# Optimization experiments

Hardware: AMD Instinct MI355X
Metric: run time of the kernel (lower is better)

## Reference

```python
import jax, jax.numpy as jnp
import numpy as np

D_MODEL = 1024
NUM_HEADS = 16
HEAD_DIM = D_MODEL // NUM_HEADS


def setup_inputs() -> dict:
    key = jax.random.key(0)
    k_x, k_wqkv, k_bqkv, k_wout, k_bout = jax.random.split(key, 5)
    B, S = 2, 2048
    x = jax.random.normal(k_x, (B, S, D_MODEL), dtype=jnp.float32)
    # haiku Linear: y = x @ W + b, W shape [in, out]
    init_scale = 1.0 / np.sqrt(D_MODEL)
    W_qkv = jax.random.normal(k_wqkv, (D_MODEL, 3 * D_MODEL), dtype=jnp.float32) * init_scale
    b_qkv = jnp.zeros((3 * D_MODEL,), dtype=jnp.float32)
    W_out = jax.random.normal(k_wout, (D_MODEL, D_MODEL), dtype=jnp.float32) * init_scale
    b_out = jnp.zeros((D_MODEL,), dtype=jnp.float32)
    return {"x": x, "W_qkv": W_qkv, "b_qkv": b_qkv, "W_out": W_out, "b_out": b_out}


def reference(x, W_qkv, b_qkv, W_out, b_out):
    B, S, _ = x.shape
    qkv = x @ W_qkv + b_qkv                      # [B, S, 3*D]
    q, k, v = jnp.split(qkv, 3, axis=-1)         # each [B, S, D]
    # [B, S, D] -> [B, H, S, Hd]
    def heads(t):
        return t.reshape(B, S, NUM_HEADS, HEAD_DIM).transpose(0, 2, 1, 3)
    q, k, v = heads(q), heads(k), heads(v)
    scale = jnp.sqrt(jnp.float32(HEAD_DIM)).astype(x.dtype)
    attn = jnp.einsum('bhqd,bhkd->bhqk', q, k) / scale   # [B, H, S, S]
    attn = jax.nn.softmax(attn, axis=-1)
    out = jnp.einsum('bhqk,bhkd->bhqd', attn, v)          # [B, H, S, Hd]
    out = out.transpose(0, 2, 1, 3).reshape(B, S, D_MODEL)
    return out @ W_out + b_out
```

## Files before the change

kernel.cpp:

```cpp
#include <hip/hip_runtime.h>
#include <stdint.h>


#define BATCH 2
#define SEQ 2048
#define DM 1024
#define NH 16
#define HD 64
#define M_TOT 4096
#define QSCALE 0.18033688011112042f

typedef __bf16 bf16x8 __attribute__((ext_vector_type(8)));
typedef __bf16 bf16x4 __attribute__((ext_vector_type(4)));
typedef float  f32x4  __attribute__((ext_vector_type(4)));

__device__ __forceinline__ void gld_lds16(const void* g, void* l) {
    __builtin_amdgcn_global_load_lds(
        (const __attribute__((address_space(1))) uint32_t*)g,
        (__attribute__((address_space(3))) uint32_t*)l, 16, 0, 0);
}

__launch_bounds__(256)
__global__ void prep_kernel(const float* __restrict__ x,
                            const float* __restrict__ Wqkv,
                            const float* __restrict__ Wout,
                            __bf16* __restrict__ xs,
                            __bf16* __restrict__ wqt,
                            __bf16* __restrict__ wot)
{
    __shared__ float T[64][69];
    const int tid = threadIdx.x;
    const int blk = blockIdx.x;

    if (blk < 4096) {
        const int i  = blk * 256 + tid;
        const int m  = i >> 8;
        const int c4 = (i & 255) * 4;
        float4 v = *reinterpret_cast<const float4*>(&x[(size_t)m * DM + c4]);
        float a[4] = {v.x, v.y, v.z, v.w};
        bf16x4 hi, lo;
        #pragma unroll
        for (int j = 0; j < 4; ++j) {
            __bf16 h = (__bf16)a[j];
            hi[j] = h;
            lo[j] = (__bf16)(a[j] - (float)h);
        }
        *reinterpret_cast<bf16x4*>(&xs[(size_t)m * (2*DM) + c4]) = hi;
        *reinterpret_cast<bf16x4*>(&xs[(size_t)m * (2*DM) + DM + c4]) = lo;
        return;
    }

    const int bb = (blk < 4864) ? blk - 4096 : blk - 4864;
    const float* W = (blk < 4864) ? Wqkv : Wout;
    __bf16* Wt     = (blk < 4864) ? wqt  : wot;
    const int N    = (blk < 4864) ? 3 * DM : DM;
    const int k0 = (bb & 15) * 64, n0 = (bb >> 4) * 64;

    {
        const int kr = tid >> 4, c4 = (tid & 15) * 4;
        #pragma unroll
        for (int i = 0; i < 4; ++i) {
            float4 v = *reinterpret_cast<const float4*>(
                &W[(size_t)(k0 + kr + 16 * i) * N + n0 + c4]);
            *reinterpret_cast<float4*>(&T[kr + 16 * i][c4]) = v;
        }
    }
    __syncthreads();
    {
        const int n = tid >> 2, kc = (tid & 3) * 16;
        __bf16 hi[16], lo[16];
        #pragma unroll
        for (int j = 0; j < 16; ++j) {
            float v = T[kc + j][n];
            __bf16 h = (__bf16)v;
            hi[j] = h;
            lo[j] = (__bf16)(v - (float)h);
        }
        const size_t ro = (size_t)(n0 + n) * (2*DM) + k0 + kc;
        *reinterpret_cast<bf16x8*>(&Wt[ro])          = *reinterpret_cast<bf16x8*>(&hi[0]);
        *reinterpret_cast<bf16x8*>(&Wt[ro + 8])      = *reinterpret_cast<bf16x8*>(&hi[8]);
        *reinterpret_cast<bf16x8*>(&Wt[ro + DM])     = *reinterpret_cast<bf16x8*>(&lo[0]);
        *reinterpret_cast<bf16x8*>(&Wt[ro + DM + 8]) = *reinterpret_cast<bf16x8*>(&lo[8]);
    }
}

__launch_bounds__(512, 2)
__global__ void gemm_qkv_kernel(const __bf16* __restrict__ A,
                                const __bf16* __restrict__ Bt,
                                const float* __restrict__ bias,
                                __bf16* __restrict__ qs,
                                __bf16* __restrict__ khi_g,
                                __bf16* __restrict__ klo_g,
                                __bf16* __restrict__ vt_g)
{
    __shared__ __align__(16) __bf16 pool[65536];

    const int tid  = threadIdx.x;
    const int w    = tid >> 6;
    const int lane = tid & 63;
    const int n16  = lane & 15;
    const int quad = lane >> 4;

    const int wg = (blockIdx.x & 7) * 24 + (blockIdx.x >> 3);
    const int bm = (wg & 15) * 256;
    const int bn = (wg >> 4) * 256;

    const int wm = (w >> 2) * 128;
    const int wn = (w & 3) * 64;

    const int r0 = tid >> 3;
    const int c0 = ((tid & 7) ^ (r0 & 7));

    auto stage = [&](int p, int kcol, int nbuf) {
        __bf16* dst = pool + nbuf * 32768 + p * 8192;
        const __bf16* gsrc = (p < 2)
            ? A  + (size_t)(bm + p * 128) * (2*DM) + kcol
            : Bt + (size_t)(bn + (p - 2) * 128) * (2*DM) + kcol;
        gld_lds16(gsrc + (size_t)r0 * (2*DM) + c0 * 8,        dst + (size_t)tid * 8);
        gld_lds16(gsrc + (size_t)(r0 + 64) * (2*DM) + c0 * 8, dst + (size_t)(512 + tid) * 8);
    };

    const int rowA = (wm + n16) * 64;
    const int rowB = (wn + n16) * 64;
    const int sx0 = ((quad)     ^ (n16 & 7)) << 3;
    const int sx1 = ((4 + quad) ^ (n16 & 7)) << 3;

    f32x4 acc[8][4] = {};
    bf16x8 af[4][2], bf0[2][2], bf1[2][2];

    stage(0, 0, 0); stage(1, 0, 0); stage(2, 0, 0); stage(3, 0, 0);

    #pragma unroll 2
    for (int t = 0; t < 48; ++t) {
        const int buf = t & 1;
        const __bf16* bufA = pool + buf * 32768;
        const __bf16* bufB = bufA + 16384;
        const int nbuf = buf ^ 1;
        const bool pre = (t < 47);
        const int tt = t + 1;
        const int a_k = (tt < 16) ? tt * 64 : tt * 64 - DM;
        const int b_k = (tt < 32) ? tt * 64 : tt * 64 - 2 * DM;

        if (pre) {
            stage(0, a_k, nbuf);
            asm volatile("s_waitcnt vmcnt(2)" ::: "memory");
        } else {
            asm volatile("s_waitcnt vmcnt(0)" ::: "memory");
        }
        __builtin_amdgcn_s_barrier();
        __builtin_amdgcn_sched_barrier(0);
        #pragma unroll
        for (int i = 0; i < 4; ++i) {
            af[i][0] = *reinterpret_cast<const bf16x8*>(bufA + rowA + i * 1024 + sx0);
            af[i][1] = *reinterpret_cast<const bf16x8*>(bufA + rowA + i * 1024 + sx1);
        }
        #pragma unroll
        for (int j = 0; j < 2; ++j) {
            bf0[j][0] = *reinterpret_cast<const bf16x8*>(bufB + rowB + j * 1024 + sx0);
            bf0[j][1] = *reinterpret_cast<const bf16x8*>(bufB + rowB + j * 1024 + sx1);
        }
        asm volatile("s_waitcnt lgkmcnt(0)" ::: "memory");
        __builtin_amdgcn_sched_barrier(0);
        __builtin_amdgcn_s_setprio(1);
        #pragma unroll
        for (int i = 0; i < 4; ++i)
            #pragma unroll
            for (int j = 0; j < 2; ++j) {
                acc[i][j] = __builtin_amdgcn_mfma_f32_16x16x32_bf16(af[i][0], bf0[j][0], acc[i][j], 0, 0, 0);
                acc[i][j] = __builtin_amdgcn_mfma_f32_16x16x32_bf16(af[i][1], bf0[j][1], acc[i][j], 0, 0, 0);
            }
        __builtin_amdgcn_s_setprio(0);

        #pragma unroll
        for (int j = 0; j < 2; ++j) {
            bf1[j][0] = *reinterpret_cast<const bf16x8*>(bufB + rowB + (2 + j) * 1024 + sx0);
            bf1[j][1] = *reinterpret_cast<const bf16x8*>(bufB + rowB + (2 + j) * 1024 + sx1);
        }
        if (pre) stage(1, a_k, nbuf);
        __builtin_amdgcn_s_barrier();
        __builtin_amdgcn_sched_barrier(0);
        asm volatile("s_waitcnt lgkmcnt(0)" ::: "memory");
        __builtin_amdgcn_sched_barrier(0);
        __builtin_amdgcn_s_setprio(1);
        #pragma unroll
        for (int i = 0; i < 4; ++i)
            #pragma unroll
            for (int j = 0; j < 2; ++j) {
                acc[i][2 + j] = __builtin_amdgcn_mfma_f32_16x16x32_bf16(af[i][0], bf1[j][0], acc[i][2 + j], 0, 0, 0);
                acc[i][2 + j] = __builtin_amdgcn_mfma_f32_16x16x32_bf16(af[i][1], bf1[j][1], acc[i][2 + j], 0, 0, 0);
            }
        __builtin_amdgcn_s_setprio(0);

        #pragma unroll
        for (int i = 0; i < 4; ++i) {
            af[i][0] = *reinterpret_cast<const bf16x8*>(bufA + rowA + (4 + i) * 1024 + sx0);
            af[i][1] = *reinterpret_cast<const bf16x8*>(bufA + rowA + (4 + i) * 1024 + sx1);
        }
        if (pre) stage(2, b_k, nbuf);
        __builtin_amdgcn_s_barrier();
        __builtin_amdgcn_sched_barrier(0);
        asm volatile("s_waitcnt lgkmcnt(0)" ::: "memory");
        __builtin_amdgcn_sched_barrier(0);
        __builtin_amdgcn_s_setprio(1);
        #pragma unroll
        for (int i = 0; i < 4; ++i)
            #pragma unroll
            for (int j = 0; j < 2; ++j) {
                acc[4 + i][j] = __builtin_amdgcn_mfma_f32_16x16x32_bf16(af[i][0], bf0[j][0], acc[4 + i][j], 0, 0, 0);
                acc[4 + i][j] = __builtin_amdgcn_mfma_f32_16x16x32_bf16(af[i][1], bf0[j][1], acc[4 + i][j], 0, 0, 0);
            }
        __builtin_amdgcn_s_setprio(0);

        if (pre) stage(3, b_k, nbuf);
        __builtin_amdgcn_s_barrier();
        __builtin_amdgcn_sched_barrier(0);
        __builtin_amdgcn_s_setprio(1);
        #pragma unroll
        for (int i = 0; i < 4; ++i)
            #pragma unroll
            for (int j = 0; j < 2; ++j) {
                acc[4 + i][2 + j] = __builtin_amdgcn_mfma_f32_16x16x32_bf16(af[i][0], bf1[j][0], acc[4 + i][2 + j], 0, 0, 0);
                acc[4 + i][2 + j] = __builtin_amdgcn_mfma_f32_16x16x32_bf16(af[i][1], bf1[j][1], acc[4 + i][2 + j], 0, 0, 0);
            }
        __builtin_amdgcn_s_setprio(0);
    }

    __syncthreads();

    const int colb = bn + wn;
    const int part = colb >> 10;
    const int hh   = (colb & 1023) >> 6;

    float bv[4];
    #pragma unroll
    for (int j = 0; j < 4; ++j) bv[j] = bias[colb + j * 16 + n16];

    __bf16* scrH = pool + w * 4608;
    __bf16* scrL = scrH + 2304;
    const int lr = lane & 31, hc = lane >> 5;

    #pragma unroll
    for (int mi = 0; mi < 2; ++mi) {
        const int brow = bm + wm + mi * 64;
        const int b    = brow >> 11;
        const int s0   = brow & 2047;
        const int bh   = b * NH + hh;
        const int kt   = s0 >> 6;
        const size_t tb = ((size_t)bh * 32 + kt) * 4096;

        #pragma unroll
        for (int p = 0; p < 2; ++p) {
            if (part == 2) {
                #pragma unroll
                for (int jj = 0; jj < 2; ++jj) {
                    const int j = 2 * p + jj;
                    #pragma unroll
                    for (int i = 0; i < 4; ++i) {
                        bf16x4 v4;
                        #pragma unroll
                        for (int r = 0; r < 4; ++r)
                            v4[r] = (__bf16)(acc[4 * mi + i][j][r] + bv[j]);
                        *reinterpret_cast<bf16x4*>(
                            &scrH[(jj * 16 + n16) * 72 + i * 16 + quad * 4]) = v4;
                    }
                }
            } else {
                #pragma unroll
                for (int ii = 0; ii < 2; ++ii) {
                    const int i = 2 * p + ii;
                    #pragma unroll
                    for (int j = 0; j < 4; ++j) {
                        #pragma unroll
                        for (int r = 0; r < 4; ++r) {
                            float val = acc[4 * mi + i][j][r] + bv[j];
                            if (part == 0) val *= QSCALE;
                            __bf16 h = (__bf16)val;
                            const int so = (ii * 16 + quad * 4 + r) * 72 + j * 16 + n16;
                            scrH[so] = h;
                            scrL[so] = (__bf16)(val - (float)h);
                        }
                    }
                }
            }
            __syncthreads();

            if (part == 0) {
                const size_t qbase = ((size_t)bh * SEQ + s0 + 32 * p + lr) * 128;
                #pragma unroll
                for (int t = 0; t < 4; ++t) {
                    const int ch = hc * 4 + t;
                    *reinterpret_cast<bf16x8*>(&qs[qbase + ch * 8]) =
                        *reinterpret_cast<const bf16x8*>(&scrH[lr * 72 + ch * 8]);
                    *reinterpret_cast<bf16x8*>(&qs[qbase + 64 + ch * 8]) =
                        *reinterpret_cast<const bf16x8*>(&scrL[lr * 72 + ch * 8]);
                }
            } else if (part == 1) {
                const int kr = 32 * p + lr;
                #pragma unroll
                for (int t = 0; t < 4; ++t) {
                    const int ch = hc * 4 + t;
                    const int src = (ch ^ (lr & 7)) * 8;
                    *reinterpret_cast<bf16x8*>(&khi_g[tb + kr * 64 + ch * 8]) =
                        *reinterpret_cast<const bf16x8*>(&scrH[lr * 72 + src]);
                    *reinterpret_cast<bf16x8*>(&klo_g[tb + kr * 64 + ch * 8]) =
                        *reinterpret_cast<const bf16x8*>(&scrL[lr * 72 + src]);
                }
            } else {
                const int d = 32 * p + lr;
                #pragma unroll
                for (int t = 0; t < 4; ++t) {
                    const int ch = hc * 4 + t;
                    const int src = (ch ^ (lr & 7)) * 8;
                    *reinterpret_cast<bf16x8*>(&vt_g[tb + d * 64 + ch * 8]) =
                        *reinterpret_cast<const bf16x8*>(&scrH[lr * 72 + src]);
                }
            }
            __syncthreads();
        }
    }
}

__launch_bounds__(256)
__global__ void gemm_out_kernel(const __bf16* __restrict__ A,
                                const __bf16* __restrict__ Bt,
                                const float* __restrict__ bias,
                                float* __restrict__ out)
{
    __shared__ __align__(16) __bf16 AsH[128 * 32];
    __shared__ __align__(16) __bf16 AsL[128 * 32];
    __shared__ __align__(16) __bf16 BsH[64 * 32];
    __shared__ __align__(16) __bf16 BsL[64 * 32];

    const int tid  = threadIdx.x;
    const int w    = tid >> 6;
    const int lane = tid & 63;
    const int n16  = lane & 15;
    const int quad = lane >> 4;
    const int bm = blockIdx.x * 128, bn = blockIdx.y * 64;
    const int wm = (w & 1) * 64,     wn = (w >> 1) * 32;

    const int srow = tid >> 2, sc = (tid & 3) * 8;
    const __bf16* Ar = A  + (size_t)(bm + srow) * (2*DM) + sc;
    const __bf16* Br = Bt + (size_t)(bn + srow) * (2*DM) + sc;

    f32x4 acc[4][2] = {};

    for (int k0 = 0; k0 < DM; k0 += 32) {
        __syncthreads();
        gld_lds16(Ar + k0,                         &AsH[(size_t)tid * 8]);
        gld_lds16(Ar + k0 + (size_t)64*2*DM,       &AsH[(size_t)(256 + tid) * 8]);
        gld_lds16(Ar + DM + k0,                    &AsL[(size_t)tid * 8]);
        gld_lds16(Ar + DM + k0 + (size_t)64*2*DM,  &AsL[(size_t)(256 + tid) * 8]);
        gld_lds16(Br + k0,                         &BsH[(size_t)tid * 8]);
        gld_lds16(Br + DM + k0,                    &BsL[(size_t)tid * 8]);
        __syncthreads();

        bf16x8 afh[4], afl[4], bfh[2], bfl[2];
        #pragma unroll
        for (int i = 0; i < 4; ++i) {
            const int ro = (wm + i*16 + n16) * 32 + quad * 8;
            afh[i] = *reinterpret_cast<const bf16x8*>(&AsH[ro]);
            afl[i] = *reinterpret_cast<const bf16x8*>(&AsL[ro]);
        }
        #pragma unroll
        for (int j = 0; j < 2; ++j) {
            const int ro = (wn + j*16 + n16) * 32 + quad * 8;
            bfh[j] = *reinterpret_cast<const bf16x8*>(&BsH[ro]);
            bfl[j] = *reinterpret_cast<const bf16x8*>(&BsL[ro]);
        }
        #pragma unroll
        for (int i = 0; i < 4; ++i)
            #pragma unroll
            for (int j = 0; j < 2; ++j) {
                acc[i][j] = __builtin_amdgcn_mfma_f32_16x16x32_bf16(afh[i], bfh[j], acc[i][j], 0, 0, 0);
                acc[i][j] = __builtin_amdgcn_mfma_f32_16x16x32_bf16(afh[i], bfl[j], acc[i][j], 0, 0, 0);
                acc[i][j] = __builtin_amdgcn_mfma_f32_16x16x32_bf16(afl[i], bfh[j], acc[i][j], 0, 0, 0);
            }
    }

    #pragma unroll
    for (int j = 0; j < 2; ++j) {
        const int col = bn + wn + j * 16 + n16;
        const float bvv = bias[col];
        #pragma unroll
        for (int i = 0; i < 4; ++i) {
            const int row0 = bm + wm + i * 16 + quad * 4;
            #pragma unroll
            for (int r = 0; r < 4; ++r)
                out[(size_t)(row0 + r) * DM + col] = acc[i][j][r] + bvv;
        }
    }
}

__launch_bounds__(512, 1)
__global__ void flash_attn_v7_kernel(const __bf16* __restrict__ qs,
                                     const __bf16* __restrict__ khi_g,
                                     const __bf16* __restrict__ klo_g,
                                     const __bf16* __restrict__ vt_g,
                                     __bf16* __restrict__ ctx2)
{
    __shared__ __align__(16) __bf16 Khi[2][4096];
    __shared__ __align__(16) __bf16 Klo[2][4096];
    __shared__ __align__(16) __bf16 Vt [2][4096];
    __shared__ __align__(16) __bf16 Ps [16384];

    const int tid  = threadIdx.x;
    const int w    = tid >> 6;
    const int lane = tid & 63;
    const int n16  = lane & 15;
    const int quad = lane >> 4;
    const int wgid = (blockIdx.x & 7) * 32 + (blockIdx.x >> 3);
    const int bh = wgid >> 3;
    const int qt = wgid & 7;

    bf16x8 qh[2][2], ql[2][2];
    #pragma unroll
    for (int qg = 0; qg < 2; ++qg) {
        const size_t qrow =
            ((size_t)bh * SEQ + qt * 256 + w * 32 + qg * 16 + n16) * 128;
        #pragma unroll
        for (int s2 = 0; s2 < 2; ++s2) {
            qh[qg][s2] = *reinterpret_cast<const bf16x8*>(&qs[qrow + s2 * 32 + quad * 8]);
            ql[qg][s2] = *reinterpret_cast<const bf16x8*>(&qs[qrow + 64 + s2 * 32 + quad * 8]);
        }
    }

    f32x4 o[2][4] = {};
    float l_lane[2] = {};

    for (int kt2 = 0; kt2 < 16; ++kt2) {
        __syncthreads();
        {
            const int buf = w >> 2;
            const size_t tb = ((size_t)bh * 32 + kt2 * 2 + buf) * 4096;
            #pragma unroll
            for (int t = 0; t < 6; ++t) {
                const int rem = (w & 3) * 6 + t;
                const int arr = rem >> 3, sub = rem & 7;
                const int eo = sub * 512 + lane * 8;
                const __bf16* g = (arr == 0 ? khi_g : arr == 1 ? klo_g : vt_g) + tb + eo;
                __bf16* l = (arr == 0 ? Khi[buf] : arr == 1 ? Klo[buf] : Vt[buf]) + eo;
                gld_lds16(g, l);
            }
        }
        __syncthreads();

        #pragma unroll
        for (int hf = 0; hf < 2; ++hf) {
            const __bf16* KhiB = Khi[hf];
            const __bf16* KloB = Klo[hf];
            const __bf16* VtB  = Vt[hf];

            #pragma unroll
            for (int kg = 0; kg < 4; ++kg) {
                const int r = kg * 16 + n16;
                const int o0 = r * 64 + ((quad ^ (r & 7)) << 3);
                const int o1 = r * 64 + (((4 + quad) ^ (r & 7)) << 3);
                bf16x8 kh0 = *reinterpret_cast<const bf16x8*>(&KhiB[o0]);
                bf16x8 kl0 = *reinterpret_cast<const bf16x8*>(&KloB[o0]);
                bf16x8 kh1 = *reinterpret_cast<const bf16x8*>(&KhiB[o1]);
                bf16x8 kl1 = *reinterpret_cast<const bf16x8*>(&KloB[o1]);
                #pragma unroll
                for (int qg = 0; qg < 2; ++qg) {
                    f32x4 sa = {}, sb = {};
                    sa = __builtin_amdgcn_mfma_f32_16x16x32_bf16(kh0, qh[qg][0], sa, 0, 0, 0);
                    sb = __builtin_amdgcn_mfma_f32_16x16x32_bf16(kh1, qh[qg][1], sb, 0, 0, 0);
                    sa = __builtin_amdgcn_mfma_f32_16x16x32_bf16(kl0, qh[qg][0], sa, 0, 0, 0);
                    sb = __builtin_amdgcn_mfma_f32_16x16x32_bf16(kl1, qh[qg][1], sb, 0, 0, 0);
                    sa = __builtin_amdgcn_mfma_f32_16x16x32_bf16(kh0, ql[qg][0], sa, 0, 0, 0);
                    sb = __builtin_amdgcn_mfma_f32_16x16x32_bf16(kh1, ql[qg][1], sb, 0, 0, 0);
                    f32x4 st = sa + sb;

                    f32x4 pp;
                    #pragma unroll
                    for (int r2 = 0; r2 < 4; ++r2) pp[r2] = exp2f(st[r2]);
                    l_lane[qg] += (pp[0] + pp[1]) + (pp[2] + pp[3]);

                    bf16x4 p4;
                    #pragma unroll
                    for (int r2 = 0; r2 < 4; ++r2) p4[r2] = (__bf16)pp[r2];
                    const int prow = w * 32 + qg * 16 + n16;
                    const int ch2 = kg * 2 + (quad >> 1);
                    const int off = prow * 64 + ((ch2 ^ (prow & 7)) << 3) + (quad & 1) * 4;
                    *reinterpret_cast<bf16x4*>(&Ps[off]) = p4;
                }
            }

            bf16x8 pa[2][2];
            #pragma unroll
            for (int qg = 0; qg < 2; ++qg) {
                const int prow = w * 32 + qg * 16 + n16;
                #pragma unroll
                for (int s2 = 0; s2 < 2; ++s2)
                    pa[qg][s2] = *reinterpret_cast<const bf16x8*>(
                        &Ps[prow * 64 + (((s2 * 4 + quad) ^ (prow & 7)) << 3)]);
            }
            #pragma unroll
            for (int c = 0; c < 4; ++c) {
                const int vr = c * 16 + n16;
                bf16x8 vb0 = *reinterpret_cast<const bf16x8*>(
                    &VtB[vr * 64 + ((quad ^ (vr & 7)) << 3)]);
                bf16x8 vb1 = *reinterpret_cast<const bf16x8*>(
                    &VtB[vr * 64 + (((4 + quad) ^ (vr & 7)) << 3)]);
                #pragma unroll
                for (int qg = 0; qg < 2; ++qg) {
                    o[qg][c] = __builtin_amdgcn_mfma_f32_16x16x32_bf16(pa[qg][0], vb0, o[qg][c], 0, 0, 0);
                    o[qg][c] = __builtin_amdgcn_mfma_f32_16x16x32_bf16(pa[qg][1], vb1, o[qg][c], 0, 0, 0);
                }
            }
        }
    }

    #pragma unroll
    for (int qg = 0; qg < 2; ++qg) {
        l_lane[qg] += __shfl_xor(l_lane[qg], 16, 64);
        l_lane[qg] += __shfl_xor(l_lane[qg], 32, 64);
    }

    const int b = bh >> 4, hh = bh & 15;
    #pragma unroll
    for (int qg = 0; qg < 2; ++qg) {
        #pragma unroll
        for (int r2 = 0; r2 < 4; ++r2) {
            const float l = __shfl(l_lane[qg], (quad << 4) + quad * 4 + r2, 64);
            const float linv = 1.0f / l;
            const int srow = qt * 256 + w * 32 + qg * 16 + quad * 4 + r2;
            const size_t rowoff = (size_t)(b * SEQ + srow) * (2*DM);
            #pragma unroll
            for (int c = 0; c < 4; ++c) {
                const int col = hh * HD + c * 16 + n16;
                float v = o[qg][c][r2] * linv;
                __bf16 h = (__bf16)v;
                ctx2[rowoff + col] = h;
                ctx2[rowoff + DM + col] = (__bf16)(v - (float)h);
            }
        }
    }
}

extern "C" void kernel_launch(void* const* d_in, const int* in_sizes, int n_in,
                              void* d_out, int out_size, void* d_ws, size_t ws_size,
                              hipStream_t stream)
{
    const float* x    = (const float*)d_in[0];
    const float* Wqkv = (const float*)d_in[1];
    const float* bqkv = (const float*)d_in[2];
    const float* Wout = (const float*)d_in[3];
    const float* bout = (const float*)d_in[4];
    float* out = (float*)d_out;

    char* ws = (char*)d_ws;
    __bf16* xs   = (__bf16*)(ws);
    __bf16* ctx2 = xs;
    __bf16* wqt  = (__bf16*)(ws + (size_t)16 * 1024 * 1024);
    __bf16* wot  = (__bf16*)(ws + (size_t)28 * 1024 * 1024);
    __bf16* qsb  = (__bf16*)(ws + (size_t)32 * 1024 * 1024);
    __bf16* khi  = (__bf16*)(ws + (size_t)48 * 1024 * 1024);
    __bf16* klo  = (__bf16*)(ws + (size_t)56 * 1024 * 1024);
    __bf16* vt   = (__bf16*)(ws + (size_t)64 * 1024 * 1024);

    prep_kernel<<<dim3(5120), 256, 0, stream>>>(x, Wqkv, Wout, xs, wqt, wot);
    gemm_qkv_kernel<<<dim3(192), 512, 0, stream>>>(
        xs, wqt, bqkv, qsb, khi, klo, vt);
    flash_attn_v7_kernel<<<dim3(256), 512, 0, stream>>>(qsb, khi, klo, vt, ctx2);
    gemm_out_kernel<<<dim3(M_TOT / 128, DM / 64), 256, 0, stream>>>(
        ctx2, wot, bout, out);
}
```

Baseline: 285.2 us.

## Rewrite output projection GEMM with 128x128 tiles and double-buffered LDS pipeline

After: 304.3 us. +6.7%, slower.

```diff
diff --git a/kernel.cpp b/kernel.cpp
--- a/kernel.cpp
+++ b/kernel.cpp
@@ -320,62 +320,127 @@
     }
 }
 
-__launch_bounds__(256)
+__launch_bounds__(512, 2)
 __global__ void gemm_out_kernel(const __bf16* __restrict__ A,
                                 const __bf16* __restrict__ Bt,
                                 const float* __restrict__ bias,
                                 float* __restrict__ out)
 {
-    __shared__ __align__(16) __bf16 AsH[128 * 32];
-    __shared__ __align__(16) __bf16 AsL[128 * 32];
-    __shared__ __align__(16) __bf16 BsH[64 * 32];
-    __shared__ __align__(16) __bf16 BsL[64 * 32];
+    __shared__ __align__(16) __bf16 pool[32768];
 
     const int tid  = threadIdx.x;
     const int w    = tid >> 6;
     const int lane = tid & 63;
     const int n16  = lane & 15;
     const int quad = lane >> 4;
-    const int bm = blockIdx.x * 128, bn = blockIdx.y * 64;
-    const int wm = (w & 1) * 64,     wn = (w >> 1) * 32;
-
-    const int srow = tid >> 2, sc = (tid & 3) * 8;
-    const __bf16* Ar = A  + (size_t)(bm + srow) * (2*DM) + sc;
-    const __bf16* Br = Bt + (size_t)(bn + srow) * (2*DM) + sc;
+
+    const int wg = (blockIdx.x & 7) * 32 + (blockIdx.x >> 3);
+    const int bm = (wg & 31) * 128;
+    const int bn = (wg >> 5) * 128;
+
+    const int wm = (w >> 2) * 64;
+    const int wn = (w & 3) * 32;
+
+    const int r0 = tid >> 3;
+    const int c0 = ((tid & 7) ^ (r0 & 7));
+
+    auto stage = [&](int p, int kcol, int nbuf) {
+        __bf16* dst = pool + nbuf * 16384 + p * 4096;
+        const __bf16* gsrc = (p < 2)
+            ? A  + (size_t)(bm + p * 64) * (2*DM) + kcol
+            : Bt + (size_t)(bn + (p - 2) * 64) * (2*DM) + kcol;
+        gld_lds16(gsrc + (size_t)r0 * (2*DM) + c0 * 8, dst + (size_t)tid * 8);
+    };
+
+    const int rowA = (wm + n16) * 64;
+    const int rowB = (wn + n16) * 64;
+    const int sx0 = ((quad)     ^ (n16 & 7)) << 3;
+    const int sx1 = ((4 + quad) ^ (n16 & 7)) << 3;
 
     f32x4 acc[4][2] = {};
-
-    for (int k0 = 0; k0 < DM; k0 += 32) {
-        __syncthreads();
-        gld_lds16(Ar + k0,                         &AsH[(size_t)tid * 8]);
-        gld_lds16(Ar + k0 + (size_t)64*2*DM,       &AsH[(size_t)(256 + tid) * 8]);
-        gld_lds16(Ar + DM + k0,                    &AsL[(size_t)tid * 8]);
-        gld_lds16(Ar + DM + k0 + (size_t)64*2*DM,  &AsL[(size_t)(256 + tid) * 8]);
-        gld_lds16(Br + k0,                         &BsH[(size_t)tid * 8]);
-        gld_lds16(Br + DM + k0,                    &BsL[(size_t)tid * 8]);
-        __syncthreads();
-
-        bf16x8 afh[4], afl[4], bfh[2], bfl[2];
-        #pragma unroll
-        for (int i = 0; i < 4; ++i) {
-            const int ro = (wm + i*16 + n16) * 32 + quad * 8;
-            afh[i] = *reinterpret_cast<const bf16x8*>(&AsH[ro]);
-            afl[i] = *reinterpret_cast<const bf16x8*>(&AsL[ro]);
-        }
-        #pragma unroll
-        for (int j = 0; j < 2; ++j) {
-            const int ro = (wn + j*16 + n16) * 32 + quad * 8;
-            bfh[j] = *reinterpret_cast<const bf16x8*>(&BsH[ro]);
-            bfl[j] = *reinterpret_cast<const bf16x8*>(&BsL[ro]);
-        }
-        #pragma unroll
-        for (int i = 0; i < 4; ++i)
-            #pragma unroll
-            for (int j = 0; j < 2; ++j) {
-                acc[i][j] = __builtin_amdgcn_mfma_f32_16x16x32_bf16(afh[i], bfh[j], acc[i][j], 0, 0, 0);
-                acc[i][j] = __builtin_amdgcn_mfma_f32_16x16x32_bf16(afh[i], bfl[j], acc[i][j], 0, 0, 0);
-                acc[i][j] = __builtin_amdgcn_mfma_f32_16x16x32_bf16(afl[i], bfh[j], acc[i][j], 0, 0, 0);
-            }
+    bf16x8 af[4][2], bf0[2], bf1[2];
+
+    stage(0, 0, 0); stage(1, 0, 0); stage(2, 0, 0); stage(3, 0, 0);
+
+    #pragma unroll 2
+    for (int t = 0; t < 48; ++t) {
+        const int buf = t & 1;
+        const __bf16* bufA = pool + buf * 16384;
+        const __bf16* bufB = bufA + 8192;
+        const int nbuf = buf ^ 1;
+        const bool pre = (t < 47);
+        const int tt = t + 1;
+        const int a_k = (tt < 16) ? tt * 64 : tt * 64 - DM;
+        const int b_k = (tt < 32) ? tt * 64 : tt * 64 - 2 * DM;
+
+        if (pre) {
+            stage(0, a_k, nbuf);
+            asm volatile("s_waitcnt vmcnt(1)" ::: "memory");
+        } else {
+            asm volatile("s_waitcnt vmcnt(0)" ::: "memory");
+        }
+        __builtin_amdgcn_s_barrier();
+        __builtin_amdgcn_sched_barrier(0);
+        #pragma unroll
+        for (int i = 0; i < 2; ++i) {
+            af[i][0] = *reinterpret_cast<const bf16x8*>(bufA + rowA + i * 1024 + sx0);
+            af[i][1] = *reinterpret_cast<const bf16x8*>(bufA + rowA + i * 1024 + sx1);
+        }
+        bf0[0] = *reinterpret_cast<const bf16x8*>(bufB + rowB + sx0);
+        bf0[1] = *reinterpret_cast<const bf16x8*>(bufB + rowB + sx1);
+        asm volatile("s_waitcnt lgkmcnt(0)" ::: "memory");
+        __builtin_amdgcn_sched_barrier(0);
+        __builtin_amdgcn_s_setprio(1);
+        #pragma unroll
+        for (int i = 0; i < 2; ++i) {
+            acc[i][0] = __builtin_amdgcn_mfma_f32_16x16x32_bf16(af[i][0], bf0[0], acc[i][0], 0, 0, 0);
+            acc[i][0] = __builtin_amdgcn_mfma_f32_16x16x32_bf16(af[i][1], bf0[1], acc[i][0], 0, 0, 0);
+        }
+        __builtin_amdgcn_s_setprio(0);
+
+        bf1[0] = *reinterpret_cast<const bf16x8*>(bufB + rowB + 1024 + sx0);
+        bf1[1] = *reinterpret_cast<const bf16x8*>(bufB + rowB + 1024 + sx1);
+        if (pre) stage(1, a_k, nbuf);
+        __builtin_amdgcn_s_barrier();
+        __builtin_amdgcn_sched_barrier(0);
+        asm volatile("s_waitcnt lgkmcnt(0)" ::: "memory");
+        __builtin_amdgcn_sched_barrier(0);
+        __builtin_amdgcn_s_setprio(1);
+        #pragma unroll
+        for (int i = 0; i < 2; ++i) {
+            acc[i][1] = __builtin_amdgcn_mfma_f32_16x16x32_bf16(af[i][0], bf1[0], acc[i][1], 0, 0, 0);
+            acc[i][1] = __builtin_amdgcn_mfma_f32_16x16x32_bf16(af[i][1], bf1[1], acc[i][1], 0, 0, 0);
+        }
+        __builtin_amdgcn_s_setprio(0);
+
+        #pragma unroll
+        for (int i = 0; i < 2; ++i) {
+            af[2 + i][0] = *reinterpret_cast<const bf16x8*>(bufA + rowA + (2 + i) * 1024 + sx0);
+            af[2 + i][1] = *reinterpret_cast<const bf16x8*>(bufA + rowA + (2 + i) * 1024 + sx1);
+        }
+        if (pre) stage(2, b_k, nbuf);
+        __builtin_amdgcn_s_barrier();
+        __builtin_amdgcn_sched_barrier(0);
+        asm volatile("s_waitcnt lgkmcnt(0)" ::: "memory");
+        __builtin_amdgcn_sched_barrier(0);
+        __builtin_amdgcn_s_setprio(1);
+        #pragma unroll
+        for (int i = 0; i < 2; ++i) {
+            acc[2 + i][0] = __builtin_amdgcn_mfma_f32_16x16x32_bf16(af[2 + i][0], bf0[0], acc[2 + i][0], 0, 0, 0);
+            acc[2 + i][0] = __builtin_amdgcn_mfma_f32_16x16x32_bf16(af[2 + i][1], bf0[1], acc[2 + i][0], 0, 0, 0);
+        }
+        __builtin_amdgcn_s_setprio(0);
+
+        if (pre) stage(3, b_k, nbuf);
+        __builtin_amdgcn_s_barrier();
+        __builtin_amdgcn_sched_barrier(0);
+        __builtin_amdgcn_s_setprio(1);
+        #pragma unroll
+        for (int i = 0; i < 2; ++i) {
+            acc[2 + i][1] = __builtin_amdgcn_mfma_f32_16x16x32_bf16(af[2 + i][0], bf1[0], acc[2 + i][1], 0, 0, 0);
+            acc[2 + i][1] = __builtin_amdgcn_mfma_f32_16x16x32_bf16(af[2 + i][1], bf1[1], acc[2 + i][1], 0, 0, 0);
+        }
+        __builtin_amdgcn_s_setprio(0);
     }
 
     #pragma unroll
@@ -563,6 +628,6 @@
     gemm_qkv_kernel<<<dim3(192), 512, 0, stream>>>(
         xs, wqt, bqkv, qsb, khi, klo, vt);
     flash_attn_v7_kernel<<<dim3(256), 512, 0, stream>>>(qsb, khi, klo, vt, ctx2);
-    gemm_out_kernel<<<dim3(M_TOT / 128, DM / 64), 256, 0, stream>>>(
+    gemm_out_kernel<<<dim3(256), 512, 0, stream>>>(
         ctx2, wot, bout, out);
 }
```
